# Performance work log

Measured on AMD Instinct MI355X. Metric: run time of the kernel, lower is better.

## Reference

```python
import jax, jax.numpy as jnp
import numpy as np

B, T, D, H = 2, 2048, 1024, 16
DK = D // H


def setup_inputs() -> dict:
    key = jax.random.key(0)
    ks = jax.random.split(key, 11)
    s = 1.0 / np.sqrt(D)
    return {
        "x_q": jax.random.normal(ks[0], (B, T, D), jnp.float32),
        "x_kv": jax.random.normal(ks[1], (B, T, D), jnp.float32),
        "mask": jnp.ones((B, 1, T, T), jnp.int32),
        "Wq": jax.random.normal(ks[2], (D, D), jnp.float32) * s,
        "bq": jnp.zeros((D,), jnp.float32),
        "Wk": jax.random.normal(ks[3], (D, D), jnp.float32) * s,
        "bk": jnp.zeros((D,), jnp.float32),
        "Wv": jax.random.normal(ks[4], (D, D), jnp.float32) * s,
        "bv": jnp.zeros((D,), jnp.float32),
        "Wo": jax.random.normal(ks[5], (D, D), jnp.float32) * s,
        "bo": jnp.zeros((D,), jnp.float32),
    }


def _split_heads(x):
    # (B, T, D) -> (B, H, T, DK)
    b, t, _ = x.shape
    return x.reshape(b, t, H, DK).transpose(0, 2, 1, 3)


def reference(x_q, x_kv, mask, Wq, bq, Wk, bk, Wv, bv, Wo, bo):
    # Linear layers use torch convention: y = x @ W.T + b
    Q = _split_heads(x_q @ Wq.T + bq)   # (B,H,Tq,DK)
    K = _split_heads(x_kv @ Wk.T + bk)  # (B,H,Tk,DK)
    V = _split_heads(x_kv @ Wv.T + bv)  # (B,H,Tk,DK)

    scores = jnp.einsum("bhqd,bhkd->bhqk", Q, K) / jnp.sqrt(jnp.float32(DK))
    scores = jnp.where(mask == 0, jnp.float32(-jnp.inf), scores)
    attn = jax.nn.softmax(scores, axis=-1)  # (B,H,Tq,Tk)

    out = jnp.einsum("bhqk,bhkd->bhqd", attn, V)
    out = out.transpose(0, 2, 1, 3).reshape(B, T, D)  # combine heads
    out = out @ Wo.T + bo
    return out, attn
```

## Files before the change

kernel.cpp:

```cpp
#include <hip/hip_runtime.h>
#include <hip/hip_bf16.h>

#define DEVINL __device__ __forceinline__

typedef __attribute__((ext_vector_type(4))) float f32x4;
typedef __attribute__((ext_vector_type(8))) short short8;
typedef __attribute__((ext_vector_type(4))) short short4v;

constexpr int CB = 2, CT = 2048, CD = 1024, CH = 16, CDK = 64;
constexpr int CM = CB * CT;
constexpr float LOG2E = 1.44269504088896340736f;

DEVINL ushort f2bf(float f) {
  __hip_bfloat16 h = __float2bfloat16(f);
  ushort u; __builtin_memcpy(&u, &h, 2); return u;
}

DEVINL void gl2lds16(const ushort* g, ushort* ldsbase) {
  __builtin_amdgcn_global_load_lds(
      (const __attribute__((address_space(1))) void*)g,
      (__attribute__((address_space(3))) void*)ldsbase, 16, 0, 0);
}

__global__ void cvt_all_kernel(const float* __restrict__ s0, ushort* __restrict__ d0, int n0,
                               const float* __restrict__ s1, ushort* __restrict__ d1, int n1,
                               const float* __restrict__ s2, ushort* __restrict__ d2, int n2,
                               const float* __restrict__ s3, ushort* __restrict__ d3, int n3,
                               const float* __restrict__ s4, ushort* __restrict__ d4, int n4,
                               const float* __restrict__ s5, ushort* __restrict__ d5, int n5)
{
  int i = (blockIdx.x * blockDim.x + threadIdx.x) * 4;
  const float* s; ushort* d;
  if (i < n0) { s = s0; d = d0; }
  else if ((i -= n0) < n1) { s = s1; d = d1; }
  else if ((i -= n1) < n2) { s = s2; d = d2; }
  else if ((i -= n2) < n3) { s = s3; d = d3; }
  else if ((i -= n3) < n4) { s = s4; d = d4; }
  else if ((i -= n4) < n5) { s = s5; d = d5; }
  else return;
  float4 v = *reinterpret_cast<const float4*>(s + i);
  ushort4 o;
  o.x = f2bf(v.x); o.y = f2bf(v.y); o.z = f2bf(v.z); o.w = f2bf(v.w);
  *reinterpret_cast<ushort4*>(d + i) = o;
}

__global__ void mask_flags_kernel(const int* __restrict__ mask, uint* __restrict__ flags) {
  const int tile = blockIdx.x;
  const int b = tile >> 10, qb = (tile >> 5) & 31, kb = tile & 31;
  const int* base = mask + ((size_t)b * CT + qb * 64) * CT + kb * 64;
  const int r = threadIdx.x >> 2, c0 = (threadIdx.x & 3) * 16;
  int ok = 1;
  for (int j = 0; j < 4; ++j) {
    int4 v = *reinterpret_cast<const int4*>(base + (size_t)r * CT + c0 + j * 4);
    ok &= (v.x != 0) & (v.y != 0) & (v.z != 0) & (v.w != 0);
  }
  __shared__ int red[4];
  unsigned long long bal = __ballot(ok);
  if ((threadIdx.x & 63) == 0) red[threadIdx.x >> 6] = (bal == ~0ull);
  __syncthreads();
  if (threadIdx.x == 0) flags[tile] = (uint)(red[0] & red[1] & red[2] & red[3]);
}

__global__ __launch_bounds__(256, 2)
void gemm_nt_kernel(const ushort* __restrict__ A, const ushort* __restrict__ Bm,
                    const float* __restrict__ bias1, const float* __restrict__ bias2,
                    void* __restrict__ Out, void* __restrict__ Out2,
                    int M, int N, int K, int mode, float scale)
{
  constexpr int BM = 128, BN = 64, BK = 32;
  __shared__ __align__(16) ushort As[2][BM * BK];
  __shared__ __align__(16) ushort Bs[2][BN * BK];
  const int tid = threadIdx.x;
  const int lane = tid & 63, wid = tid >> 6;
  const int wr = wid >> 1, wc = wid & 1;
  const int bm0 = blockIdx.y * BM, bn0 = blockIdx.x * BN;
  const int rsel = lane & 15, ksel = (lane >> 4) * 8;
  const int srow = lane >> 2, sc8 = (lane & 3) * 8;

  f32x4 acc[4][2];
  for (int i = 0; i < 4; ++i) for (int j = 0; j < 2; ++j) acc[i][j] = f32x4{0.f, 0.f, 0.f, 0.f};

  auto stage = [&](int bu, int k0) {
    const int ra0 = wid * 32;
    gl2lds16(&A[(size_t)(bm0 + ra0 + srow) * K + k0 + sc8],      &As[bu][ra0 * BK]);
    gl2lds16(&A[(size_t)(bm0 + ra0 + 16 + srow) * K + k0 + sc8], &As[bu][(ra0 + 16) * BK]);
    const int rb0 = wid * 16;
    gl2lds16(&Bm[(size_t)(bn0 + rb0 + srow) * K + k0 + sc8],     &Bs[bu][rb0 * BK]);
  };

  stage(0, 0);
  __syncthreads();
  const int NKT = K / BK;
  int bu = 0;
  for (int kt = 0; kt < NKT; ++kt) {
    if (kt + 1 < NKT) stage(bu ^ 1, (kt + 1) * BK);
    short8 af[4], bfr[2];
    for (int mi = 0; mi < 4; ++mi)
      af[mi] = *reinterpret_cast<short8*>(&As[bu][(wr * 64 + mi * 16 + rsel) * BK + ksel]);
    for (int ni = 0; ni < 2; ++ni)
      bfr[ni] = *reinterpret_cast<short8*>(&Bs[bu][(wc * 32 + ni * 16 + rsel) * BK + ksel]);
    for (int mi = 0; mi < 4; ++mi)
      for (int ni = 0; ni < 2; ++ni)
        acc[mi][ni] = __builtin_amdgcn_mfma_f32_16x16x32_bf16(af[mi], bfr[ni], acc[mi][ni], 0, 0, 0);
    if (kt + 1 < NKT) { __syncthreads(); bu ^= 1; }
  }

  const int r0 = (lane >> 4) * 4;
  for (int mi = 0; mi < 4; ++mi)
    for (int ni = 0; ni < 2; ++ni) {
      int gj = bn0 + wc * 32 + ni * 16 + rsel;
      float bv = (mode == 3 && gj >= 1024) ? bias2[gj - 1024] : bias1[gj];
      for (int r = 0; r < 4; ++r) {
        int gi = bm0 + wr * 64 + mi * 16 + r0 + r;
        float v = (acc[mi][ni][r] + bv) * scale;
        if (mode == 2) {
          reinterpret_cast<float*>(Out)[(size_t)gi * N + gj] = v;
        } else {
          int bb = gi >> 11, t = gi & (CT - 1);
          if (mode == 3 && gj >= 1024) {
            int gjv = gj - 1024;
            reinterpret_cast<ushort*>(Out2)[(((size_t)(bb * CH + (gjv >> 6)) * CDK + (gjv & 63)) * CT + t)] = f2bf(v);
          } else {
            reinterpret_cast<ushort*>(Out)[(((size_t)(bb * CH + (gj >> 6)) * CT + t) * CDK + (gj & 63))] = f2bf(v);
          }
        }
      }
    }
}

__global__ __launch_bounds__(512, 2)
void attn_kernel(const ushort* __restrict__ Qb, const ushort* __restrict__ Kb,
                 const ushort* __restrict__ Vt, const int* __restrict__ mask,
                 const uint* __restrict__ flags,
                 float* __restrict__ attn_out, ushort* __restrict__ oh)
{
  constexpr int LDP = 72;
  __shared__ __align__(16) ushort Ks[2][64 * 64];
  __shared__ __align__(16) ushort Vs[2][64 * 64];
  __shared__ __align__(16) ushort Ps[8][16 * LDP];

  const int tid = threadIdx.x, wid = tid >> 6, lane = tid & 63;
  const int bh = blockIdx.y, b = bh >> 4, h = bh & 15;
  const int q0 = blockIdx.x * 128 + wid * 16;
  const int rsel = lane & 15, grp = lane >> 4, ksel = grp * 8;
  const int swz = rsel & 7;
  const uint* fl = flags + (b << 10) + ((q0 >> 6) << 5);
  const ushort* kpan = Kb + (size_t)bh * CT * CDK;
  const ushort* vpan = Vt + (size_t)bh * CDK * CT;

  const int strow = tid >> 3, stc = (tid & 7) ^ (strow & 7);

  auto stageK = [&](int bu, int k0) {
    gl2lds16(&kpan[(size_t)(k0 + strow) * CDK + stc * 8], &Ks[bu][(size_t)wid * 512]);
  };
  auto stageV = [&](int bu, int k0) {
    gl2lds16(&vpan[(size_t)strow * CT + k0 + stc * 8], &Vs[bu][(size_t)wid * 512]);
  };

  short8 qa0, qa1;
  {
    const ushort* qrow = Qb + ((size_t)bh * CT + q0 + rsel) * CDK;
    qa0 = *reinterpret_cast<const short8*>(qrow + ksel);
    qa1 = *reinterpret_cast<const short8*>(qrow + 32 + ksel);
  }

  const int* mrow = mask + (size_t)b * CT * CT;
  const int qme = q0 + rsel;

  float l_lane = 0.f;
  stageK(0, 0);
  __syncthreads();
  int bu = 0;
  for (int kt = 0; kt < 32; ++kt) {
    const int k0 = kt * 64;
    if (kt + 1 < 32) stageK(bu ^ 1, k0 + 64);
    const uint f = fl[kt];
    for (int ni = 0; ni < 4; ++ni) {
      const int krow = ni * 16 + rsel;
      short8 kb0 = *reinterpret_cast<short8*>(&Ks[bu][krow * 64 + ((grp    ) ^ swz) * 8]);
      short8 kb1 = *reinterpret_cast<short8*>(&Ks[bu][krow * 64 + ((grp + 4) ^ swz) * 8]);
      f32x4 z = {0.f, 0.f, 0.f, 0.f};
      z = __builtin_amdgcn_mfma_f32_16x16x32_bf16(kb0, qa0, z, 0, 0, 0);
      z = __builtin_amdgcn_mfma_f32_16x16x32_bf16(kb1, qa1, z, 0, 0, 0);
      if (f) {
        l_lane += exp2f(z[0]) + exp2f(z[1]) + exp2f(z[2]) + exp2f(z[3]);
      } else {
        const int kb_ = k0 + ni * 16 + grp * 4;
        for (int r = 0; r < 4; ++r)
          l_lane += mrow[(size_t)qme * CT + kb_ + r] ? exp2f(z[r]) : 0.f;
      }
    }
    __syncthreads();
    bu ^= 1;
  }
  l_lane += __shfl_xor(l_lane, 16, 64);
  l_lane += __shfl_xor(l_lane, 32, 64);
  const float inv_l = 1.f / l_lane;

  f32x4 oacc[4];
  for (int nd = 0; nd < 4; ++nd) oacc[nd] = f32x4{0.f, 0.f, 0.f, 0.f};
  float* aq = attn_out + (size_t)bh * CT * CT + (size_t)qme * CT;
  ushort* pw = &Ps[wid][0];

  stageK(0, 0);
  stageV(0, 0);
  __syncthreads();
  bu = 0;
  for (int kt = 0; kt < 32; ++kt) {
    const int k0 = kt * 64;
    if (kt + 1 < 32) { stageK(bu ^ 1, k0 + 64); stageV(bu ^ 1, k0 + 64); }
    const uint f = fl[kt];
    for (int ni = 0; ni < 4; ++ni) {
      const int krow = ni * 16 + rsel;
      short8 kb0 = *reinterpret_cast<short8*>(&Ks[bu][krow * 64 + ((grp    ) ^ swz) * 8]);
      short8 kb1 = *reinterpret_cast<short8*>(&Ks[bu][krow * 64 + ((grp + 4) ^ swz) * 8]);
      f32x4 z = {0.f, 0.f, 0.f, 0.f};
      z = __builtin_amdgcn_mfma_f32_16x16x32_bf16(kb0, qa0, z, 0, 0, 0);
      z = __builtin_amdgcn_mfma_f32_16x16x32_bf16(kb1, qa1, z, 0, 0, 0);
      const int kb_ = k0 + ni * 16 + grp * 4;
      float p0, p1, p2, p3;
      if (f) {
        p0 = exp2f(z[0]); p1 = exp2f(z[1]); p2 = exp2f(z[2]); p3 = exp2f(z[3]);
      } else {
        const size_t mb = (size_t)qme * CT + kb_;
        p0 = mrow[mb + 0] ? exp2f(z[0]) : 0.f;
        p1 = mrow[mb + 1] ? exp2f(z[1]) : 0.f;
        p2 = mrow[mb + 2] ? exp2f(z[2]) : 0.f;
        p3 = mrow[mb + 3] ? exp2f(z[3]) : 0.f;
      }
      float4 st = make_float4(p0 * inv_l, p1 * inv_l, p2 * inv_l, p3 * inv_l);
      *reinterpret_cast<float4*>(aq + kb_) = st;
      short4v pk = {(short)f2bf(p0), (short)f2bf(p1), (short)f2bf(p2), (short)f2bf(p3)};
      *reinterpret_cast<short4v*>(&pw[rsel * LDP + ni * 16 + grp * 4]) = pk;
    }
    short8 pa0 = *reinterpret_cast<short8*>(&pw[rsel * LDP + ksel]);
    short8 pa1 = *reinterpret_cast<short8*>(&pw[rsel * LDP + 32 + ksel]);
    for (int nd = 0; nd < 4; ++nd) {
      const int vrow = nd * 16 + rsel;
      short8 vb0 = *reinterpret_cast<short8*>(&Vs[bu][vrow * 64 + ((grp    ) ^ swz) * 8]);
      short8 vb1 = *reinterpret_cast<short8*>(&Vs[bu][vrow * 64 + ((grp + 4) ^ swz) * 8]);
      oacc[nd] = __builtin_amdgcn_mfma_f32_16x16x32_bf16(pa0, vb0, oacc[nd], 0, 0, 0);
      oacc[nd] = __builtin_amdgcn_mfma_f32_16x16x32_bf16(pa1, vb1, oacc[nd], 0, 0, 0);
    }
    __syncthreads();
    bu ^= 1;
  }

  float invl_o[4];
  for (int r = 0; r < 4; ++r) invl_o[r] = __shfl(inv_l, grp * 4 + r, 16);
  for (int nd = 0; nd < 4; ++nd)
    for (int r = 0; r < 4; ++r) {
      int q = q0 + grp * 4 + r, d = nd * 16 + rsel;
      oh[((size_t)b * CT + q) * CD + h * CDK + d] = f2bf(oacc[nd][r] * invl_o[r]);
    }
}

extern "C" void kernel_launch(void* const* d_in, const int* in_sizes, int n_in,
                              void* d_out, int out_size, void* d_ws, size_t ws_size,
                              hipStream_t stream)
{
  const float* x_q  = (const float*)d_in[0];
  const float* x_kv = (const float*)d_in[1];
  const int*   mask = (const int*)d_in[2];
  const float* Wq = (const float*)d_in[3];
  const float* bq = (const float*)d_in[4];
  const float* Wk = (const float*)d_in[5];
  const float* bk = (const float*)d_in[6];
  const float* Wv = (const float*)d_in[7];
  const float* bv = (const float*)d_in[8];
  const float* Wo = (const float*)d_in[9];
  const float* bo = (const float*)d_in[10];

  float* out  = (float*)d_out;
  float* attn = out + (size_t)CB * CT * CD;

  char* w = (char*)d_ws;
  auto alloc = [&](size_t bytes) { char* p = w; w += (bytes + 255) & ~(size_t)255; return p; };
  ushort* xq_bf  = (ushort*)alloc((size_t)CM * CD * 2);
  ushort* xkv_bf = (ushort*)alloc((size_t)CM * CD * 2);
  ushort* Wq_bf  = (ushort*)alloc((size_t)CD * CD * 2);
  ushort* Wk_bf  = (ushort*)alloc((size_t)CD * CD * 2);
  ushort* Wv_bf  = (ushort*)alloc((size_t)CD * CD * 2);
  ushort* Wo_bf  = (ushort*)alloc((size_t)CD * CD * 2);
  ushort* Q_bf   = (ushort*)alloc((size_t)CM * CD * 2);
  ushort* K_bf   = (ushort*)alloc((size_t)CM * CD * 2);
  ushort* Vt_bf  = (ushort*)alloc((size_t)CM * CD * 2);
  ushort* oh_bf  = (ushort*)alloc((size_t)CM * CD * 2);
  uint*   mflags = (uint*)alloc(2048 * sizeof(uint));

  {
    const int nx = CM * CD, nw = CD * CD;
    const int total_quads = (2 * nx + 4 * nw) / 4;
    const int blocks = (total_quads + 255) / 256;
    hipLaunchKernelGGL(cvt_all_kernel, dim3(blocks), dim3(256), 0, stream,
                       x_q, xq_bf, nx, x_kv, xkv_bf, nx,
                       Wq, Wq_bf, nw, Wk, Wk_bf, nw,
                       Wv, Wv_bf, nw, Wo, Wo_bf, nw);
  }

  hipLaunchKernelGGL(mask_flags_kernel, dim3(2048), dim3(256), 0, stream, mask, mflags);

  hipLaunchKernelGGL(gemm_nt_kernel, dim3(CD / 64, CM / 128), dim3(256), 0, stream,
                     xq_bf, Wq_bf, bq, bq, (void*)Q_bf, nullptr, CM, CD, CD, 0, 0.125f * LOG2E);
  hipLaunchKernelGGL(gemm_nt_kernel, dim3(2 * CD / 64, CM / 128), dim3(256), 0, stream,
                     xkv_bf, Wk_bf, bk, bv, (void*)K_bf, (void*)Vt_bf, CM, 2 * CD, CD, 3, 1.0f);

  hipLaunchKernelGGL(attn_kernel, dim3(CT / 128, CB * CH), dim3(512), 0, stream,
                     Q_bf, K_bf, Vt_bf, mask, mflags, attn, oh_bf);

  hipLaunchKernelGGL(gemm_nt_kernel, dim3(CD / 64, CM / 128), dim3(256), 0, stream,
                     oh_bf, Wo_bf, bo, bo, d_out, nullptr, CM, CD, CD, 2, 1.0f);
}
```

Before: 330.7 us.

## Stage normalized probabilities in LDS as fp32 for coalesced nontemporal attn stores

```diff
diff --git a/kernel.cpp b/kernel.cpp
--- a/kernel.cpp
+++ b/kernel.cpp
@@ -5,7 +5,6 @@
 
 typedef __attribute__((ext_vector_type(4))) float f32x4;
 typedef __attribute__((ext_vector_type(8))) short short8;
-typedef __attribute__((ext_vector_type(4))) short short4v;
 
 constexpr int CB = 2, CT = 2048, CD = 1024, CH = 16, CDK = 64;
 constexpr int CM = CB * CT;
@@ -134,10 +133,9 @@
                  const uint* __restrict__ flags,
                  float* __restrict__ attn_out, ushort* __restrict__ oh)
 {
-  constexpr int LDP = 72;
   __shared__ __align__(16) ushort Ks[2][64 * 64];
   __shared__ __align__(16) ushort Vs[2][64 * 64];
-  __shared__ __align__(16) ushort Ps[8][16 * LDP];
+  __shared__ __align__(16) float  Pf[8][16 * 64];
 
   const int tid = threadIdx.x, wid = tid >> 6, lane = tid & 63;
   const int bh = blockIdx.y, b = bh >> 4, h = bh & 15;
@@ -195,12 +193,12 @@
   }
   l_lane += __shfl_xor(l_lane, 16, 64);
   l_lane += __shfl_xor(l_lane, 32, 64);
-  const float inv_l = 1.f / l_lane;
+  const float ll = __log2f(l_lane);
 
   f32x4 oacc[4];
   for (int nd = 0; nd < 4; ++nd) oacc[nd] = f32x4{0.f, 0.f, 0.f, 0.f};
-  float* aq = attn_out + (size_t)bh * CT * CT + (size_t)qme * CT;
-  ushort* pw = &Ps[wid][0];
+  float* apan = attn_out + (size_t)bh * CT * CT;
+  float* pf = &Pf[wid][0];
 
   stageK(0, 0);
   stageV(0, 0);
@@ -217,24 +215,34 @@
       f32x4 z = {0.f, 0.f, 0.f, 0.f};
       z = __builtin_amdgcn_mfma_f32_16x16x32_bf16(kb0, qa0, z, 0, 0, 0);
       z = __builtin_amdgcn_mfma_f32_16x16x32_bf16(kb1, qa1, z, 0, 0, 0);
-      const int kb_ = k0 + ni * 16 + grp * 4;
       float p0, p1, p2, p3;
       if (f) {
-        p0 = exp2f(z[0]); p1 = exp2f(z[1]); p2 = exp2f(z[2]); p3 = exp2f(z[3]);
+        p0 = exp2f(z[0] - ll); p1 = exp2f(z[1] - ll);
+        p2 = exp2f(z[2] - ll); p3 = exp2f(z[3] - ll);
       } else {
-        const size_t mb = (size_t)qme * CT + kb_;
-        p0 = mrow[mb + 0] ? exp2f(z[0]) : 0.f;
-        p1 = mrow[mb + 1] ? exp2f(z[1]) : 0.f;
-        p2 = mrow[mb + 2] ? exp2f(z[2]) : 0.f;
-        p3 = mrow[mb + 3] ? exp2f(z[3]) : 0.f;
+        const size_t mb = (size_t)qme * CT + k0 + ni * 16 + grp * 4;
+        p0 = mrow[mb + 0] ? exp2f(z[0] - ll) : 0.f;
+        p1 = mrow[mb + 1] ? exp2f(z[1] - ll) : 0.f;
+        p2 = mrow[mb + 2] ? exp2f(z[2] - ll) : 0.f;
+        p3 = mrow[mb + 3] ? exp2f(z[3] - ll) : 0.f;
       }
-      float4 st = make_float4(p0 * inv_l, p1 * inv_l, p2 * inv_l, p3 * inv_l);
-      *reinterpret_cast<float4*>(aq + kb_) = st;
-      short4v pk = {(short)f2bf(p0), (short)f2bf(p1), (short)f2bf(p2), (short)f2bf(p3)};
-      *reinterpret_cast<short4v*>(&pw[rsel * LDP + ni * 16 + grp * 4]) = pk;
-    }
-    short8 pa0 = *reinterpret_cast<short8*>(&pw[rsel * LDP + ksel]);
-    short8 pa1 = *reinterpret_cast<short8*>(&pw[rsel * LDP + 32 + ksel]);
+      *reinterpret_cast<f32x4*>(&pf[rsel * 64 + (((ni * 4 + grp) ^ swz) << 2)]) =
+          f32x4{p0, p1, p2, p3};
+    }
+    for (int rr = 0; rr < 4; ++rr) {
+      const int row = rr * 4 + grp;
+      f32x4 v = *reinterpret_cast<f32x4*>(&pf[row * 64 + ((rsel ^ (row & 7)) << 2)]);
+      __builtin_nontemporal_store(v,
+          reinterpret_cast<f32x4*>(apan + (size_t)(q0 + row) * CT + k0 + rsel * 4));
+    }
+    f32x4 a0 = *reinterpret_cast<f32x4*>(&pf[rsel * 64 + (((2 * grp    ) ^ swz) << 2)]);
+    f32x4 a1 = *reinterpret_cast<f32x4*>(&pf[rsel * 64 + (((2 * grp + 1) ^ swz) << 2)]);
+    f32x4 a2 = *reinterpret_cast<f32x4*>(&pf[rsel * 64 + (((2 * grp + 8) ^ swz) << 2)]);
+    f32x4 a3 = *reinterpret_cast<f32x4*>(&pf[rsel * 64 + (((2 * grp + 9) ^ swz) << 2)]);
+    short8 pa0 = {(short)f2bf(a0[0]), (short)f2bf(a0[1]), (short)f2bf(a0[2]), (short)f2bf(a0[3]),
+                  (short)f2bf(a1[0]), (short)f2bf(a1[1]), (short)f2bf(a1[2]), (short)f2bf(a1[3])};
+    short8 pa1 = {(short)f2bf(a2[0]), (short)f2bf(a2[1]), (short)f2bf(a2[2]), (short)f2bf(a2[3]),
+                  (short)f2bf(a3[0]), (short)f2bf(a3[1]), (short)f2bf(a3[2]), (short)f2bf(a3[3])};
     for (int nd = 0; nd < 4; ++nd) {
       const int vrow = nd * 16 + rsel;
       short8 vb0 = *reinterpret_cast<short8*>(&Vs[bu][vrow * 64 + ((grp    ) ^ swz) * 8]);
@@ -246,12 +254,10 @@
     bu ^= 1;
   }
 
-  float invl_o[4];
-  for (int r = 0; r < 4; ++r) invl_o[r] = __shfl(inv_l, grp * 4 + r, 16);
   for (int nd = 0; nd < 4; ++nd)
     for (int r = 0; r < 4; ++r) {
       int q = q0 + grp * 4 + r, d = nd * 16 + rsel;
-      oh[((size_t)b * CT + q) * CD + h * CDK + d] = f2bf(oacc[nd][r] * invl_o[r]);
+      oh[((size_t)b * CT + q) * CD + h * CDK + d] = f2bf(oacc[nd][r]);
     }
 }
 
```

New measurement: 283.6 us. -14.2%, faster.
